# Kernel optimization log

Hardware: AMD Instinct MI355X
Metric: run time of the kernel (lower is better)

Reference implementation:

```python
import jax, jax.numpy as jnp
from jax import lax
import numpy as np


def setup_inputs() -> dict:
    key = jax.random.key(0)
    ks = jax.random.split(key, 9)
    B, T, H = 64, 4096, 128
    G = 4 * H
    s = 1.0 / np.sqrt(H)  # PyTorch LSTM default init scale
    return {
        "data": jax.random.normal(ks[0], (B, T, 1), dtype=jnp.float32),
        "h0": jax.random.normal(ks[1], (B, H), dtype=jnp.float32),
        "c0": jax.random.normal(ks[2], (B, H), dtype=jnp.float32),
        "W_ih": jax.random.uniform(ks[3], (G, 1), jnp.float32, -s, s),
        "W_hh": jax.random.uniform(ks[4], (G, H), jnp.float32, -s, s),
        "b_ih": jax.random.uniform(ks[5], (G,), jnp.float32, -s, s),
        "b_hh": jax.random.uniform(ks[6], (G,), jnp.float32, -s, s),
        "W_out": jax.random.uniform(ks[7], (1, H), jnp.float32, -s, s),
        "b_out": jax.random.uniform(ks[8], (1,), jnp.float32, -s, s),
    }


def reference(data, h0, c0, W_ih, W_hh, b_ih, b_hh, W_out, b_out):
    # Single-layer batch-first LSTM (PyTorch gate order i,f,g,o), then Linear on last step.
    H = h0.shape[-1]
    # Precompute input projections for all timesteps: [B, T, 4H] -> time-major [T, B, 4H]
    x_proj = jnp.einsum("bti,gi->btg", data, W_ih) + b_ih + b_hh
    x_proj = jnp.swapaxes(x_proj, 0, 1)

    def step(carry, xg):
        h, c = carry
        gates = xg + h @ W_hh.T  # [B, 4H]
        i = jax.nn.sigmoid(gates[:, 0 * H:1 * H])
        f = jax.nn.sigmoid(gates[:, 1 * H:2 * H])
        g = jnp.tanh(gates[:, 2 * H:3 * H])
        o = jax.nn.sigmoid(gates[:, 3 * H:4 * H])
        c = f * c + i * g
        h = o * jnp.tanh(c)
        return (h, c), None

    (hT, _), _ = lax.scan(step, (h0, c0), x_proj)
    # out[:, -1, :] of the LSTM is hT; final linear projection -> [B, 1]
    return hT @ W_out.T + b_out
```

## Files before the change

### kernel.cpp

```cpp
#include <hip/hip_runtime.h>
#include <math.h>

constexpr int Hdim = 128;
constexpr int TMAX = 4096;

typedef _Float16 v8h __attribute__((ext_vector_type(8)));
typedef float v4f __attribute__((ext_vector_type(4)));

#if __has_builtin(__builtin_amdgcn_exp2f)
__device__ __forceinline__ float exp2_fast(float x) {
  return __builtin_amdgcn_exp2f(x);
}
#else
__device__ __forceinline__ float exp2_fast(float x) {
  return __expf(x * 0.6931471805599453f);
}
#endif

__device__ __forceinline__ float sel4(v4f d, int r) {
  const float s01 = (r & 1) ? d.y : d.x;
  const float s23 = (r & 1) ? d.w : d.z;
  return (r & 2) ? s23 : s01;
}

__global__ __launch_bounds__(512) void lstm_mfma(
    const float* __restrict__ data, const float* __restrict__ h0,
    const float* __restrict__ c0, const float* __restrict__ W_ih,
    const float* __restrict__ W_hh, const float* __restrict__ b_ih,
    const float* __restrict__ b_hh, const float* __restrict__ W_out,
    const float* __restrict__ b_out, float* __restrict__ out, int T) {
  __shared__ __align__(16) float xs[TMAX];
  __shared__ __align__(16) _Float16 hbuf[2][Hdim];

  const int b = blockIdx.x;
  const int tid = threadIdx.x;
  const int lane = tid & 63;
  const int wv = tid >> 6;
  const int p = lane >> 4;
  const int m = lane & 15;
  const int r = m & 3;
  const int el = 16 * wv + 4 * p + r;

  {
    const float4* src = (const float4*)(data + (size_t)b * T);
    float4* dst = (float4*)xs;
    for (int i = tid; i < T / 4; i += 512) dst[i] = src[i];
  }

  constexpr float L2E = 1.44269504088896f;

  v8h a[4][4];
#pragma unroll
  for (int g = 0; g < 4; ++g) {
    const int row = 128 * g + 16 * wv + m;
    const float Mr = (g == 2) ? 2.0f * L2E : -L2E;
    const float* wr = W_hh + (size_t)row * Hdim + 8 * p;
#pragma unroll
    for (int c = 0; c < 4; ++c) {
      float4 v0 = ((const float4*)(wr + 32 * c))[0];
      float4 v1 = ((const float4*)(wr + 32 * c))[1];
      a[g][c] = v8h{(_Float16)(Mr * v0.x), (_Float16)(Mr * v0.y),
                    (_Float16)(Mr * v0.z), (_Float16)(Mr * v0.w),
                    (_Float16)(Mr * v1.x), (_Float16)(Mr * v1.y),
                    (_Float16)(Mr * v1.z), (_Float16)(Mr * v1.w)};
    }
  }

  v4f acc_init[4];
#pragma unroll
  for (int g = 0; g < 4; ++g) {
    const float Mr = (g == 2) ? 2.0f * L2E : -L2E;
    const int row = 128 * g + 16 * wv + 4 * p;
    acc_init[g] = v4f{Mr * (b_ih[row + 0] + b_hh[row + 0]),
                      Mr * (b_ih[row + 1] + b_hh[row + 1]),
                      Mr * (b_ih[row + 2] + b_hh[row + 2]),
                      Mr * (b_ih[row + 3] + b_hh[row + 3])};
  }

  float wih[4];
#pragma unroll
  for (int g = 0; g < 4; ++g) {
    const float Mr = (g == 2) ? 2.0f * L2E : -L2E;
    wih[g] = Mr * W_ih[128 * g + el];
  }

  float cst = c0[(size_t)b * Hdim + el];
  if (tid < 128) hbuf[0][tid] = (_Float16)h0[(size_t)b * Hdim + tid];
  __syncthreads();

  for (int t0 = 0; t0 < T; t0 += 4) {
    const float4 xv = *(const float4*)&xs[t0];
    const float xts[4] = {xv.x, xv.y, xv.z, xv.w};
#pragma unroll
    for (int u = 0; u < 4; ++u) {
      const int t = t0 + u;
      const _Float16* hb = hbuf[t & 1];
      _Float16* hn = hbuf[(t + 1) & 1];
      v8h bq[4];
#pragma unroll
      for (int c = 0; c < 4; ++c) bq[c] = *(const v8h*)(hb + 32 * c + 8 * p);
      const float xt = xts[u];

      v4f d0 = __builtin_amdgcn_mfma_f32_16x16x32_f16(a[0][0], bq[0],
                                                      acc_init[0], 0, 0, 0);
      v4f d1 = __builtin_amdgcn_mfma_f32_16x16x32_f16(a[1][0], bq[0],
                                                      acc_init[1], 0, 0, 0);
      v4f d2 = __builtin_amdgcn_mfma_f32_16x16x32_f16(a[2][0], bq[0],
                                                      acc_init[2], 0, 0, 0);
      v4f d3 = __builtin_amdgcn_mfma_f32_16x16x32_f16(a[3][0], bq[0],
                                                      acc_init[3], 0, 0, 0);
#pragma unroll
      for (int c = 1; c < 4; ++c) {
        d0 = __builtin_amdgcn_mfma_f32_16x16x32_f16(a[0][c], bq[c], d0, 0, 0, 0);
        d1 = __builtin_amdgcn_mfma_f32_16x16x32_f16(a[1][c], bq[c], d1, 0, 0, 0);
        d2 = __builtin_amdgcn_mfma_f32_16x16x32_f16(a[2][c], bq[c], d2, 0, 0, 0);
        d3 = __builtin_amdgcn_mfma_f32_16x16x32_f16(a[3][c], bq[c], d3, 0, 0, 0);
      }

      const float zi = sel4(d0, r);
      const float zf = sel4(d1, r);
      const float zg = sel4(d2, r);
      const float zo = sel4(d3, r);

      const float yi =
          __builtin_amdgcn_rcpf(1.0f + exp2_fast(fmaf(xt, wih[0], zi)));
      const float yf =
          __builtin_amdgcn_rcpf(1.0f + exp2_fast(fmaf(xt, wih[1], zf)));
      const float yg = fmaf(
          -2.0f, __builtin_amdgcn_rcpf(1.0f + exp2_fast(fmaf(xt, wih[2], zg))),
          1.0f);
      const float yo =
          __builtin_amdgcn_rcpf(1.0f + exp2_fast(fmaf(xt, wih[3], zo)));

      cst = fmaf(yf, cst, yi * yg);
      const float th = fmaf(
          -2.0f, __builtin_amdgcn_rcpf(1.0f + exp2_fast(cst * (2.0f * L2E))),
          1.0f);
      const float h = yo * th;

      if (m < 4) hn[el] = (_Float16)h;
      __syncthreads();
    }
  }

  if (tid < 64) {
    const _Float16* hf = hbuf[T & 1];
    float sum =
        (float)hf[tid] * W_out[tid] + (float)hf[tid + 64] * W_out[tid + 64];
#pragma unroll
    for (int off = 32; off > 0; off >>= 1) sum += __shfl_down(sum, off, 64);
    if (tid == 0) out[b] = sum + b_out[0];
  }
}

extern "C" void kernel_launch(void* const* d_in, const int* in_sizes, int n_in,
                              void* d_out, int out_size, void* d_ws,
                              size_t ws_size, hipStream_t stream) {
  const float* data = (const float*)d_in[0];
  const float* h0 = (const float*)d_in[1];
  const float* c0 = (const float*)d_in[2];
  const float* W_ih = (const float*)d_in[3];
  const float* W_hh = (const float*)d_in[4];
  const float* b_ih = (const float*)d_in[5];
  const float* b_hh = (const float*)d_in[6];
  const float* W_out = (const float*)d_in[7];
  const float* b_out = (const float*)d_in[8];
  float* out = (float*)d_out;

  const int B = in_sizes[1] / Hdim;
  const int T = in_sizes[0] / B;

  lstm_mfma<<<B, 512, 0, stream>>>(data, h0, c0, W_ih, W_hh, b_ih, b_hh,
                                   W_out, b_out, out, T);
}
```

Before: 1.689 ms.

## Replace MFMA gate matvec with per-thread fp16 dot2 rows and DPP gate exchange

Each thread now owns one gate row of W_hh, held as 64 packed fp16 pairs in registers, and computes its 128-long dot product with the broadcast hidden state using fdot2 over eight independent accumulators. The four gates of a hidden element sit in adjacent lanes and are exchanged with quad DPP permutes, so no MFMA or result-lane selection is needed. The goal is to shorten the per-timestep serial latency of the recurrent step. In exchange every thread reads the full hidden vector from LDS each step, and register pressure is high because of the 64 weight registers and the launch_bounds(512,2) limit.

```diff
diff --git a/kernel.cpp b/kernel.cpp
--- a/kernel.cpp
+++ b/kernel.cpp
@@ -4,8 +4,8 @@
 constexpr int Hdim = 128;
 constexpr int TMAX = 4096;
 
+typedef _Float16 v2h __attribute__((ext_vector_type(2)));
 typedef _Float16 v8h __attribute__((ext_vector_type(8)));
-typedef float v4f __attribute__((ext_vector_type(4)));
 
 #if __has_builtin(__builtin_amdgcn_exp2f)
 __device__ __forceinline__ float exp2_fast(float x) {
@@ -17,13 +17,30 @@
 }
 #endif
 
-__device__ __forceinline__ float sel4(v4f d, int r) {
-  const float s01 = (r & 1) ? d.y : d.x;
-  const float s23 = (r & 1) ? d.w : d.z;
-  return (r & 2) ? s23 : s01;
+__device__ __forceinline__ float rcp_fast(float x) {
+  return __builtin_amdgcn_rcpf(x);
 }
 
-__global__ __launch_bounds__(512) void lstm_mfma(
+__device__ __forceinline__ float dot2f(v2h a, v2h b, float c) {
+#if __has_builtin(__builtin_amdgcn_fdot2)
+  return __builtin_amdgcn_fdot2(a, b, c, false);
+#else
+  return fmaf((float)a[0], (float)b[0], fmaf((float)a[1], (float)b[1], c));
+#endif
+}
+
+template <int CTRL>
+__device__ __forceinline__ float qperm(float v) {
+#if __has_builtin(__builtin_amdgcn_update_dpp)
+  return __int_as_float(
+      __builtin_amdgcn_update_dpp(0, __float_as_int(v), CTRL, 0xF, 0xF, true));
+#else
+  const int x = (CTRL == 0xB1) ? 1 : (CTRL == 0x4E ? 2 : 3);
+  return __shfl_xor(v, x, 64);
+#endif
+}
+
+__global__ __launch_bounds__(512, 2) void lstm_dot(
     const float* __restrict__ data, const float* __restrict__ h0,
     const float* __restrict__ c0, const float* __restrict__ W_ih,
     const float* __restrict__ W_hh, const float* __restrict__ b_ih,
@@ -34,12 +51,9 @@
 
   const int b = blockIdx.x;
   const int tid = threadIdx.x;
-  const int lane = tid & 63;
-  const int wv = tid >> 6;
-  const int p = lane >> 4;
-  const int m = lane & 15;
-  const int r = m & 3;
-  const int el = 16 * wv + 4 * p + r;
+  const int g = tid & 3;
+  const int el = tid >> 2;
+  const int row = 128 * g + el;
 
   {
     const float4* src = (const float4*)(data + (size_t)b * T);
@@ -48,41 +62,21 @@
   }
 
   constexpr float L2E = 1.44269504088896f;
+  const float Mr = (g == 2) ? 2.0f * L2E : -L2E;
 
-  v8h a[4][4];
+  v2h wp[64];
+  {
+    const float* wr = W_hh + (size_t)row * Hdim;
 #pragma unroll
-  for (int g = 0; g < 4; ++g) {
-    const int row = 128 * g + 16 * wv + m;
-    const float Mr = (g == 2) ? 2.0f * L2E : -L2E;
-    const float* wr = W_hh + (size_t)row * Hdim + 8 * p;
-#pragma unroll
-    for (int c = 0; c < 4; ++c) {
-      float4 v0 = ((const float4*)(wr + 32 * c))[0];
-      float4 v1 = ((const float4*)(wr + 32 * c))[1];
-      a[g][c] = v8h{(_Float16)(Mr * v0.x), (_Float16)(Mr * v0.y),
-                    (_Float16)(Mr * v0.z), (_Float16)(Mr * v0.w),
-                    (_Float16)(Mr * v1.x), (_Float16)(Mr * v1.y),
-                    (_Float16)(Mr * v1.z), (_Float16)(Mr * v1.w)};
+    for (int i = 0; i < 32; ++i) {
+      float4 v = ((const float4*)wr)[i];
+      wp[2 * i] = v2h{(_Float16)(Mr * v.x), (_Float16)(Mr * v.y)};
+      wp[2 * i + 1] = v2h{(_Float16)(Mr * v.z), (_Float16)(Mr * v.w)};
     }
   }
 
-  v4f acc_init[4];
-#pragma unroll
-  for (int g = 0; g < 4; ++g) {
-    const float Mr = (g == 2) ? 2.0f * L2E : -L2E;
-    const int row = 128 * g + 16 * wv + 4 * p;
-    acc_init[g] = v4f{Mr * (b_ih[row + 0] + b_hh[row + 0]),
-                      Mr * (b_ih[row + 1] + b_hh[row + 1]),
-                      Mr * (b_ih[row + 2] + b_hh[row + 2]),
-                      Mr * (b_ih[row + 3] + b_hh[row + 3])};
-  }
-
-  float wih[4];
-#pragma unroll
-  for (int g = 0; g < 4; ++g) {
-    const float Mr = (g == 2) ? 2.0f * L2E : -L2E;
-    wih[g] = Mr * W_ih[128 * g + el];
-  }
+  const float bias_s = Mr * (b_ih[row] + b_hh[row]);
+  const float wih_s = Mr * W_ih[row];
 
   float cst = c0[(size_t)b * Hdim + el];
   if (tid < 128) hbuf[0][tid] = (_Float16)h0[(size_t)b * Hdim + tid];
@@ -96,49 +90,42 @@
       const int t = t0 + u;
       const _Float16* hb = hbuf[t & 1];
       _Float16* hn = hbuf[(t + 1) & 1];
-      v8h bq[4];
+
+      v8h hv[16];
 #pragma unroll
-      for (int c = 0; c < 4; ++c) bq[c] = *(const v8h*)(hb + 32 * c + 8 * p);
-      const float xt = xts[u];
+      for (int i = 0; i < 16; ++i) hv[i] = *(const v8h*)(hb + 8 * i);
 
-      v4f d0 = __builtin_amdgcn_mfma_f32_16x16x32_f16(a[0][0], bq[0],
-                                                      acc_init[0], 0, 0, 0);
-      v4f d1 = __builtin_amdgcn_mfma_f32_16x16x32_f16(a[1][0], bq[0],
-                                                      acc_init[1], 0, 0, 0);
-      v4f d2 = __builtin_amdgcn_mfma_f32_16x16x32_f16(a[2][0], bq[0],
-                                                      acc_init[2], 0, 0, 0);
-      v4f d3 = __builtin_amdgcn_mfma_f32_16x16x32_f16(a[3][0], bq[0],
-                                                      acc_init[3], 0, 0, 0);
+      float a0 = bias_s, a1 = 0.f, a2 = 0.f, a3 = 0.f, a4 = 0.f, a5 = 0.f,
+            a6 = 0.f, a7 = 0.f;
 #pragma unroll
-      for (int c = 1; c < 4; ++c) {
-        d0 = __builtin_amdgcn_mfma_f32_16x16x32_f16(a[0][c], bq[c], d0, 0, 0, 0);
-        d1 = __builtin_amdgcn_mfma_f32_16x16x32_f16(a[1][c], bq[c], d1, 0, 0, 0);
-        d2 = __builtin_amdgcn_mfma_f32_16x16x32_f16(a[2][c], bq[c], d2, 0, 0, 0);
-        d3 = __builtin_amdgcn_mfma_f32_16x16x32_f16(a[3][c], bq[c], d3, 0, 0, 0);
+      for (int i = 0; i < 8; ++i) {
+        const v8h hA = hv[2 * i];
+        const v8h hB = hv[2 * i + 1];
+        a0 = dot2f(wp[8 * i + 0], v2h{hA[0], hA[1]}, a0);
+        a1 = dot2f(wp[8 * i + 1], v2h{hA[2], hA[3]}, a1);
+        a2 = dot2f(wp[8 * i + 2], v2h{hA[4], hA[5]}, a2);
+        a3 = dot2f(wp[8 * i + 3], v2h{hA[6], hA[7]}, a3);
+        a4 = dot2f(wp[8 * i + 4], v2h{hB[0], hB[1]}, a4);
+        a5 = dot2f(wp[8 * i + 5], v2h{hB[2], hB[3]}, a5);
+        a6 = dot2f(wp[8 * i + 6], v2h{hB[4], hB[5]}, a6);
+        a7 = dot2f(wp[8 * i + 7], v2h{hB[6], hB[7]}, a7);
       }
+      const float dsum = ((a0 + a1) + (a2 + a3)) + ((a4 + a5) + (a6 + a7));
 
-      const float zi = sel4(d0, r);
-      const float zf = sel4(d1, r);
-      const float zg = sel4(d2, r);
-      const float zo = sel4(d3, r);
+      const float z = fmaf(xts[u], wih_s, dsum);
+      const float uu = rcp_fast(1.0f + exp2_fast(z));
 
-      const float yi =
-          __builtin_amdgcn_rcpf(1.0f + exp2_fast(fmaf(xt, wih[0], zi)));
-      const float yf =
-          __builtin_amdgcn_rcpf(1.0f + exp2_fast(fmaf(xt, wih[1], zf)));
-      const float yg = fmaf(
-          -2.0f, __builtin_amdgcn_rcpf(1.0f + exp2_fast(fmaf(xt, wih[2], zg))),
-          1.0f);
-      const float yo =
-          __builtin_amdgcn_rcpf(1.0f + exp2_fast(fmaf(xt, wih[3], zo)));
+      const float x1 = qperm<0xB1>(uu);
+      const float x2 = qperm<0x4E>(uu);
+      const float x3 = qperm<0x1B>(uu);
 
-      cst = fmaf(yf, cst, yi * yg);
-      const float th = fmaf(
-          -2.0f, __builtin_amdgcn_rcpf(1.0f + exp2_fast(cst * (2.0f * L2E))),
-          1.0f);
-      const float h = yo * th;
-
-      if (m < 4) hn[el] = (_Float16)h;
+      if (g == 0) {
+        const float gg = fmaf(-2.0f, x2, 1.0f);
+        cst = fmaf(x1, cst, uu * gg);
+        const float th = fmaf(
+            -2.0f, rcp_fast(1.0f + exp2_fast(cst * (2.0f * L2E))), 1.0f);
+        hn[el] = (_Float16)(x3 * th);
+      }
       __syncthreads();
     }
   }
@@ -170,6 +157,6 @@
   const int B = in_sizes[1] / Hdim;
   const int T = in_sizes[0] / B;
 
-  lstm_mfma<<<B, 512, 0, stream>>>(data, h0, c0, W_ih, W_hh, b_ih, b_hh,
-                                   W_out, b_out, out, T);
+  lstm_dot<<<B, 512, 0, stream>>>(data, h0, c0, W_ih, W_hh, b_ih, b_hh, W_out,
+                                  b_out, out, T);
 }
```

New measurement: 2.349 ms. 39.1% more time.

## Split hidden units between MFMA waves and VALU dot2 waves

Applied to the files above, without the earlier changes.

Half the waves keep the MFMA path for hidden units 0-63, and the other four waves compute units 64-127 with per-lane fdot2 dot products over register-resident fp16 weights. Gate values are exchanged within quads via DPP permutes. The aim is to halve contention on each SIMD's matrix pipe by running matrix and vector work concurrently. The risk is that the VALU path (64 dot2 ops plus a full h broadcast read from LDS) becomes the slower critical path and raises register pressure.

```diff
diff --git a/kernel.cpp b/kernel.cpp
--- a/kernel.cpp
+++ b/kernel.cpp
@@ -4,6 +4,7 @@
 constexpr int Hdim = 128;
 constexpr int TMAX = 4096;
 
+typedef _Float16 v2h __attribute__((ext_vector_type(2)));
 typedef _Float16 v8h __attribute__((ext_vector_type(8)));
 typedef float v4f __attribute__((ext_vector_type(4)));
 
@@ -16,6 +17,21 @@
   return __expf(x * 0.6931471805599453f);
 }
 #endif
+
+__device__ __forceinline__ float rcp_fast(float x) {
+  return __builtin_amdgcn_rcpf(x);
+}
+
+__device__ __forceinline__ float dot2u(unsigned a, unsigned b, float c) {
+#if __has_builtin(__builtin_amdgcn_fdot2)
+  return __builtin_amdgcn_fdot2(__builtin_bit_cast(v2h, a),
+                                __builtin_bit_cast(v2h, b), c, false);
+#else
+  const v2h x = __builtin_bit_cast(v2h, a);
+  const v2h y = __builtin_bit_cast(v2h, b);
+  return fmaf((float)x[0], (float)y[0], fmaf((float)x[1], (float)y[1], c));
+#endif
+}
 
 __device__ __forceinline__ float sel4(v4f d, int r) {
   const float s01 = (r & 1) ? d.y : d.x;
@@ -23,7 +39,18 @@
   return (r & 2) ? s23 : s01;
 }
 
-__global__ __launch_bounds__(512) void lstm_mfma(
+template <int CTRL>
+__device__ __forceinline__ float qperm(float v) {
+#if __has_builtin(__builtin_amdgcn_update_dpp)
+  return __int_as_float(
+      __builtin_amdgcn_update_dpp(0, __float_as_int(v), CTRL, 0xF, 0xF, true));
+#else
+  const int x = (CTRL == 0xB1) ? 1 : (CTRL == 0x4E ? 2 : 3);
+  return __shfl_xor(v, x, 64);
+#endif
+}
+
+__global__ __launch_bounds__(512) void lstm_hyb(
     const float* __restrict__ data, const float* __restrict__ h0,
     const float* __restrict__ c0, const float* __restrict__ W_ih,
     const float* __restrict__ W_hh, const float* __restrict__ b_ih,
@@ -36,10 +63,7 @@
   const int tid = threadIdx.x;
   const int lane = tid & 63;
   const int wv = tid >> 6;
-  const int p = lane >> 4;
-  const int m = lane & 15;
-  const int r = m & 3;
-  const int el = 16 * wv + 4 * p + r;
+  const bool mrole = (wv < 4);
 
   {
     const float4* src = (const float4*)(data + (size_t)b * T);
@@ -50,38 +74,62 @@
   constexpr float L2E = 1.44269504088896f;
 
   v8h a[4][4];
-#pragma unroll
-  for (int g = 0; g < 4; ++g) {
-    const int row = 128 * g + 16 * wv + m;
+  v4f acc_init[4];
+  float wihm[4];
+  int p = 0, m = 0, r = 0;
+  unsigned wq[64];
+  float bias_s = 0.f, wih_s = 0.f;
+  int g = 0;
+
+  int el;
+  if (mrole) {
+    p = lane >> 4;
+    m = lane & 15;
+    r = m & 3;
+    el = 16 * wv + 4 * p + r;
+#pragma unroll
+    for (int gg = 0; gg < 4; ++gg) {
+      const int row = 128 * gg + 16 * wv + m;
+      const float Mr = (gg == 2) ? 2.0f * L2E : -L2E;
+      const float* wr = W_hh + (size_t)row * Hdim + 8 * p;
+#pragma unroll
+      for (int c = 0; c < 4; ++c) {
+        float4 v0 = ((const float4*)(wr + 32 * c))[0];
+        float4 v1 = ((const float4*)(wr + 32 * c))[1];
+        a[gg][c] = v8h{(_Float16)(Mr * v0.x), (_Float16)(Mr * v0.y),
+                       (_Float16)(Mr * v0.z), (_Float16)(Mr * v0.w),
+                       (_Float16)(Mr * v1.x), (_Float16)(Mr * v1.y),
+                       (_Float16)(Mr * v1.z), (_Float16)(Mr * v1.w)};
+      }
+    }
+#pragma unroll
+    for (int gg = 0; gg < 4; ++gg) {
+      const float Mr = (gg == 2) ? 2.0f * L2E : -L2E;
+      const int row = 128 * gg + 16 * wv + 4 * p;
+      acc_init[gg] = v4f{Mr * (b_ih[row + 0] + b_hh[row + 0]),
+                         Mr * (b_ih[row + 1] + b_hh[row + 1]),
+                         Mr * (b_ih[row + 2] + b_hh[row + 2]),
+                         Mr * (b_ih[row + 3] + b_hh[row + 3])};
+      wihm[gg] = Mr * W_ih[128 * gg + el];
+    }
+  } else {
+    const int s = wv - 4;
+    g = lane & 3;
+    const int local = lane >> 2;
+    el = 64 + 16 * s + local;
+    const int row = 128 * g + el;
     const float Mr = (g == 2) ? 2.0f * L2E : -L2E;
-    const float* wr = W_hh + (size_t)row * Hdim + 8 * p;
-#pragma unroll
-    for (int c = 0; c < 4; ++c) {
-      float4 v0 = ((const float4*)(wr + 32 * c))[0];
-      float4 v1 = ((const float4*)(wr + 32 * c))[1];
-      a[g][c] = v8h{(_Float16)(Mr * v0.x), (_Float16)(Mr * v0.y),
-                    (_Float16)(Mr * v0.z), (_Float16)(Mr * v0.w),
-                    (_Float16)(Mr * v1.x), (_Float16)(Mr * v1.y),
-                    (_Float16)(Mr * v1.z), (_Float16)(Mr * v1.w)};
-    }
-  }
-
-  v4f acc_init[4];
-#pragma unroll
-  for (int g = 0; g < 4; ++g) {
-    const float Mr = (g == 2) ? 2.0f * L2E : -L2E;
-    const int row = 128 * g + 16 * wv + 4 * p;
-    acc_init[g] = v4f{Mr * (b_ih[row + 0] + b_hh[row + 0]),
-                      Mr * (b_ih[row + 1] + b_hh[row + 1]),
-                      Mr * (b_ih[row + 2] + b_hh[row + 2]),
-                      Mr * (b_ih[row + 3] + b_hh[row + 3])};
-  }
-
-  float wih[4];
-#pragma unroll
-  for (int g = 0; g < 4; ++g) {
-    const float Mr = (g == 2) ? 2.0f * L2E : -L2E;
-    wih[g] = Mr * W_ih[128 * g + el];
+    const float* wr = W_hh + (size_t)row * Hdim;
+#pragma unroll
+    for (int i = 0; i < 32; ++i) {
+      float4 v = ((const float4*)wr)[i];
+      const v2h p0{(_Float16)(Mr * v.x), (_Float16)(Mr * v.y)};
+      const v2h p1{(_Float16)(Mr * v.z), (_Float16)(Mr * v.w)};
+      wq[2 * i] = __builtin_bit_cast(unsigned, p0);
+      wq[2 * i + 1] = __builtin_bit_cast(unsigned, p1);
+    }
+    bias_s = Mr * (b_ih[row] + b_hh[row]);
+    wih_s = Mr * W_ih[row];
   }
 
   float cst = c0[(size_t)b * Hdim + el];
@@ -96,49 +144,86 @@
       const int t = t0 + u;
       const _Float16* hb = hbuf[t & 1];
       _Float16* hn = hbuf[(t + 1) & 1];
-      v8h bq[4];
-#pragma unroll
-      for (int c = 0; c < 4; ++c) bq[c] = *(const v8h*)(hb + 32 * c + 8 * p);
       const float xt = xts[u];
 
-      v4f d0 = __builtin_amdgcn_mfma_f32_16x16x32_f16(a[0][0], bq[0],
-                                                      acc_init[0], 0, 0, 0);
-      v4f d1 = __builtin_amdgcn_mfma_f32_16x16x32_f16(a[1][0], bq[0],
-                                                      acc_init[1], 0, 0, 0);
-      v4f d2 = __builtin_amdgcn_mfma_f32_16x16x32_f16(a[2][0], bq[0],
-                                                      acc_init[2], 0, 0, 0);
-      v4f d3 = __builtin_amdgcn_mfma_f32_16x16x32_f16(a[3][0], bq[0],
-                                                      acc_init[3], 0, 0, 0);
-#pragma unroll
-      for (int c = 1; c < 4; ++c) {
-        d0 = __builtin_amdgcn_mfma_f32_16x16x32_f16(a[0][c], bq[c], d0, 0, 0, 0);
-        d1 = __builtin_amdgcn_mfma_f32_16x16x32_f16(a[1][c], bq[c], d1, 0, 0, 0);
-        d2 = __builtin_amdgcn_mfma_f32_16x16x32_f16(a[2][c], bq[c], d2, 0, 0, 0);
-        d3 = __builtin_amdgcn_mfma_f32_16x16x32_f16(a[3][c], bq[c], d3, 0, 0, 0);
+      if (mrole) {
+        v8h bq[4];
+#pragma unroll
+        for (int c = 0; c < 4; ++c) bq[c] = *(const v8h*)(hb + 32 * c + 8 * p);
+
+        v4f d0 = __builtin_amdgcn_mfma_f32_16x16x32_f16(a[0][0], bq[0],
+                                                        acc_init[0], 0, 0, 0);
+        v4f d1 = __builtin_amdgcn_mfma_f32_16x16x32_f16(a[1][0], bq[0],
+                                                        acc_init[1], 0, 0, 0);
+        v4f d2 = __builtin_amdgcn_mfma_f32_16x16x32_f16(a[2][0], bq[0],
+                                                        acc_init[2], 0, 0, 0);
+        v4f d3 = __builtin_amdgcn_mfma_f32_16x16x32_f16(a[3][0], bq[0],
+                                                        acc_init[3], 0, 0, 0);
+#pragma unroll
+        for (int c = 1; c < 4; ++c) {
+          d0 = __builtin_amdgcn_mfma_f32_16x16x32_f16(a[0][c], bq[c], d0, 0, 0, 0);
+          d1 = __builtin_amdgcn_mfma_f32_16x16x32_f16(a[1][c], bq[c], d1, 0, 0, 0);
+          d2 = __builtin_amdgcn_mfma_f32_16x16x32_f16(a[2][c], bq[c], d2, 0, 0, 0);
+          d3 = __builtin_amdgcn_mfma_f32_16x16x32_f16(a[3][c], bq[c], d3, 0, 0, 0);
+        }
+
+        const float zi = sel4(d0, r);
+        const float zf = sel4(d1, r);
+        const float zg = sel4(d2, r);
+        const float zo = sel4(d3, r);
+
+        const float yi =
+            rcp_fast(1.0f + exp2_fast(fmaf(xt, wihm[0], zi)));
+        const float yf =
+            rcp_fast(1.0f + exp2_fast(fmaf(xt, wihm[1], zf)));
+        const float yg =
+            fmaf(-2.0f, rcp_fast(1.0f + exp2_fast(fmaf(xt, wihm[2], zg))), 1.0f);
+        const float yo =
+            rcp_fast(1.0f + exp2_fast(fmaf(xt, wihm[3], zo)));
+
+        cst = fmaf(yf, cst, yi * yg);
+        const float th = fmaf(
+            -2.0f, rcp_fast(1.0f + exp2_fast(cst * (2.0f * L2E))), 1.0f);
+        const float h = yo * th;
+        if (m < 4) hn[el] = (_Float16)h;
+      } else {
+        const uint4* hp = (const uint4*)hb;
+        uint4 hq[16];
+#pragma unroll
+        for (int i = 0; i < 16; ++i) hq[i] = hp[i];
+
+        float a0 = bias_s, a1 = 0.f, a2 = 0.f, a3 = 0.f, a4 = 0.f, a5 = 0.f,
+              a6 = 0.f, a7 = 0.f;
+#pragma unroll
+        for (int i = 0; i < 8; ++i) {
+          const uint4 hA = hq[2 * i];
+          const uint4 hB = hq[2 * i + 1];
+          a0 = dot2u(wq[8 * i + 0], hA.x, a0);
+          a1 = dot2u(wq[8 * i + 1], hA.y, a1);
+          a2 = dot2u(wq[8 * i + 2], hA.z, a2);
+          a3 = dot2u(wq[8 * i + 3], hA.w, a3);
+          a4 = dot2u(wq[8 * i + 4], hB.x, a4);
+          a5 = dot2u(wq[8 * i + 5], hB.y, a5);
+          a6 = dot2u(wq[8 * i + 6], hB.z, a6);
+          a7 = dot2u(wq[8 * i + 7], hB.w, a7);
+        }
+        const float dsum = ((a0 + a1) + (a2 + a3)) + ((a4 + a5) + (a6 + a7));
+
+        const float z = fmaf(xt, wih_s, dsum);
+        const float uu = rcp_fast(1.0f + exp2_fast(z));
+
+        const float x1 = qperm<0xB1>(uu);
+        const float x2 = qperm<0x4E>(uu);
+        const float x3 = qperm<0x1B>(uu);
+
+        if (g == 0) {
+          const float gg = fmaf(-2.0f, x2, 1.0f);
+          cst = fmaf(x1, cst, uu * gg);
+          const float th = fmaf(
+              -2.0f, rcp_fast(1.0f + exp2_fast(cst * (2.0f * L2E))), 1.0f);
+          hn[el] = (_Float16)(x3 * th);
+        }
       }
-
-      const float zi = sel4(d0, r);
-      const float zf = sel4(d1, r);
-      const float zg = sel4(d2, r);
-      const float zo = sel4(d3, r);
-
-      const float yi =
-          __builtin_amdgcn_rcpf(1.0f + exp2_fast(fmaf(xt, wih[0], zi)));
-      const float yf =
-          __builtin_amdgcn_rcpf(1.0f + exp2_fast(fmaf(xt, wih[1], zf)));
-      const float yg = fmaf(
-          -2.0f, __builtin_amdgcn_rcpf(1.0f + exp2_fast(fmaf(xt, wih[2], zg))),
-          1.0f);
-      const float yo =
-          __builtin_amdgcn_rcpf(1.0f + exp2_fast(fmaf(xt, wih[3], zo)));
-
-      cst = fmaf(yf, cst, yi * yg);
-      const float th = fmaf(
-          -2.0f, __builtin_amdgcn_rcpf(1.0f + exp2_fast(cst * (2.0f * L2E))),
-          1.0f);
-      const float h = yo * th;
-
-      if (m < 4) hn[el] = (_Float16)h;
       __syncthreads();
     }
   }
@@ -170,6 +255,6 @@
   const int B = in_sizes[1] / Hdim;
   const int T = in_sizes[0] / B;
 
-  lstm_mfma<<<B, 512, 0, stream>>>(data, h0, c0, W_ih, W_hh, b_ih, b_hh,
-                                   W_out, b_out, out, T);
-}
+  lstm_hyb<<<B, 512, 0, stream>>>(data, h0, c0, W_ih, W_hh, b_ih, b_hh, W_out,
+                                  b_out, out, T);
+}
```

Measured after the change: 2.056 ms. 21.8% more time.
